# Optimization experiments

Measured on AMD Instinct MI355X. Metric: run time of the kernel, lower is better.

Reference implementation:

```python
import jax, jax.numpy as jnp
import numpy as np

N = 50000       # nodes
E = 1250000     # edges
DIM = 64
H = 16
DPH = DIM // H  # 4
LN_EPS = 1e-5


def setup_inputs() -> dict:
    key = jax.random.key(0)
    ks = jax.random.split(key, 10)
    return {
        "node_feat": jax.random.normal(ks[0], (N, DIM), jnp.float32),
        "edge_feat": jax.random.normal(ks[1], (E, H, DPH), jnp.float32),
        "node_vec": jax.random.normal(ks[2], (N, 3, DIM), jnp.float32),
        "radial": jax.random.uniform(ks[3], (E,), jnp.float32),
        "ln_g": jnp.ones((DIM,), jnp.float32),
        "ln_b": jnp.zeros((DIM,), jnp.float32),
        "qkv_w": jax.random.normal(ks[4], (DIM, 3 * DIM), jnp.float32) / np.sqrt(DIM).astype(np.float32),
        "qkv_b": jnp.zeros((3 * DIM,), jnp.float32),
        "vec_w": jax.random.normal(ks[5], (DIM, 2 * DIM), jnp.float32) / np.sqrt(DIM).astype(np.float32),
        "out_w": jax.random.normal(ks[6], (DIM, 2 * DIM), jnp.float32) / np.sqrt(DIM).astype(np.float32),
        "out_b": jnp.zeros((2 * DIM,), jnp.float32),
        "row": jax.random.randint(ks[7], (E,), 0, N, jnp.int32),
        "col": jax.random.randint(ks[8], (E,), 0, N, jnp.int32),
        "natoms": N,
    }


def reference(node_feat, edge_feat, node_vec, radial, ln_g, ln_b,
              qkv_w, qkv_b, vec_w, out_w, out_b, row, col, natoms):
    # LayerNorm (biased variance, as torch)
    mu = jnp.mean(node_feat, axis=-1, keepdims=True)
    var = jnp.mean(jnp.square(node_feat - mu), axis=-1, keepdims=True)
    x = (node_feat - mu) * jax.lax.rsqrt(var + LN_EPS) * ln_g + ln_b

    # QKV projection -> [N, H, 3*DPH], split
    qkv = (x @ qkv_w + qkv_b).reshape(-1, H, 3 * DPH)
    q = qkv[..., :DPH]
    k = qkv[..., DPH:2 * DPH]
    v = qkv[..., 2 * DPH:]

    # Gather by edge indices, gated dot-product attention per edge  [E, H]
    attn = jax.nn.gelu(jnp.sum(q[row] * k[col], axis=-1), approximate=False) * radial[:, None]

    # Equivariant vector gate  [N, DIM]
    iv = node_vec @ vec_w  # [N, 3, 2*DIM]
    input_dot = jnp.sum(iv[..., :DIM] * iv[..., DIM:], axis=-2)

    # Edge messages and scatter-add into nodes
    m = v[col] * edge_feat * attn[..., None]          # [E, H, DPH]
    m_agg = jax.ops.segment_sum(m, row, num_segments=natoms)  # [N, H, DPH]
    m_agg = m_agg.reshape(natoms, DIM)

    out = m_agg @ out_w + out_b                        # [N, 2*DIM]
    return input_dot * out[..., :DIM] + out[..., DIM:]
```

## Files before the change

### kernel.cpp

```cpp
#include <hip/hip_runtime.h>
#include <math.h>

#define DIM 64
#define NW 4
#define NPB 4
#define CAP 64
#define OVCAP 65536

__device__ __forceinline__ float waveReduceSum(float v) {
    #pragma unroll
    for (int off = 1; off < 64; off <<= 1)
        v += __shfl_xor(v, off, 64);
    return v;
}

__global__ __launch_bounds__(256) void qkv_kernel(
    const float* __restrict__ node_feat,
    const float* __restrict__ ln_g, const float* __restrict__ ln_b,
    const float* __restrict__ qkv_w, const float* __restrict__ qkv_b,
    float* __restrict__ q, float* __restrict__ k, float* __restrict__ v,
    int N)
{
    __shared__ float  wlds[64 * 192];
    __shared__ float4 xs[NW][NPB][16];
    const int wave = threadIdx.x >> 6, lane = threadIdx.x & 63;

    for (int idx = threadIdx.x; idx < 64 * 192; idx += 256) {
        int d = idx / 192, j = idx - d * 192;
        int jj = j & 63, sec = j >> 6;
        int c = 12 * (jj >> 2) + (jj & 3) + 4 * sec;
        wlds[idx] = qkv_w[d * 192 + c];
    }
    const int c0 = 12 * (lane >> 2) + (lane & 3);
    const float b0 = qkv_b[c0], b1 = qkv_b[c0 + 4], b2 = qkv_b[c0 + 8];
    const float gg = ln_g[lane], bb = ln_b[lane];
    __syncthreads();

    const int nstride = gridDim.x * NW * NPB;
    for (int n0 = (blockIdx.x * NW + wave) * NPB; n0 < N; n0 += nstride) {
        const int cnt = min(NPB, N - n0);
        float acc0[NPB], acc1[NPB], acc2[NPB];
        #pragma unroll
        for (int i = 0; i < NPB; ++i) {
            acc0[i] = b0; acc1[i] = b1; acc2[i] = b2;
            if (i < cnt) {
                float nf = node_feat[(size_t)(n0 + i) * DIM + lane];
                float mu = waveReduceSum(nf) * (1.0f / 64.0f);
                float dv = nf - mu;
                float var = waveReduceSum(dv * dv) * (1.0f / 64.0f);
                float x = dv * rsqrtf(var + 1e-5f) * gg + bb;
                ((float*)&xs[wave][i][0])[lane] = x;
            }
        }
        #pragma unroll 4
        for (int d4 = 0; d4 < 16; ++d4) {
            float4 xv[NPB];
            #pragma unroll
            for (int i = 0; i < NPB; ++i) xv[i] = xs[wave][i][d4];
            #pragma unroll
            for (int u = 0; u < 4; ++u) {
                int d = d4 * 4 + u;
                float w0 = wlds[d * 192 + lane];
                float w1 = wlds[d * 192 + lane + 64];
                float w2 = wlds[d * 192 + lane + 128];
                #pragma unroll
                for (int i = 0; i < NPB; ++i) {
                    float xd = (&xv[i].x)[u];
                    acc0[i] = fmaf(xd, w0, acc0[i]);
                    acc1[i] = fmaf(xd, w1, acc1[i]);
                    acc2[i] = fmaf(xd, w2, acc2[i]);
                }
            }
        }
        #pragma unroll
        for (int i = 0; i < NPB; ++i) if (i < cnt) {
            size_t off = (size_t)(n0 + i) * DIM + lane;
            q[off] = acc0[i]; k[off] = acc1[i]; v[off] = acc2[i];
        }
    }
}

__global__ __launch_bounds__(256) void vec_kernel(
    const float* __restrict__ node_vec,
    const float* __restrict__ vec_w,
    float* __restrict__ input_dot,
    float* __restrict__ m_agg,
    int* __restrict__ deg,
    int* __restrict__ ovcnt,
    int N)
{
    __shared__ float  vlds[64 * 128];
    __shared__ float4 nvs[NW][NPB][3][16];
    const int wave = threadIdx.x >> 6, lane = threadIdx.x & 63;

    if (blockIdx.x == 0 && threadIdx.x == 0) *ovcnt = 0;

    for (int idx = threadIdx.x; idx < 64 * 128; idx += 256)
        vlds[idx] = vec_w[idx];
    __syncthreads();

    const int nstride = gridDim.x * NW * NPB;
    for (int n0 = (blockIdx.x * NW + wave) * NPB; n0 < N; n0 += nstride) {
        const int cnt = min(NPB, N - n0);
        float a0[NPB][3], a1[NPB][3];
        #pragma unroll
        for (int i = 0; i < NPB; ++i) {
            #pragma unroll
            for (int s = 0; s < 3; ++s) {
                a0[i][s] = 0.f; a1[i][s] = 0.f;
                if (i < cnt)
                    ((float*)&nvs[wave][i][s][0])[lane] =
                        node_vec[((size_t)(n0 + i) * 3 + s) * DIM + lane];
            }
        }
        #pragma unroll 2
        for (int d4 = 0; d4 < 16; ++d4) {
            #pragma unroll
            for (int u = 0; u < 4; ++u) {
                int d = d4 * 4 + u;
                float w0 = vlds[d * 128 + lane];
                float w1 = vlds[d * 128 + lane + 64];
                #pragma unroll
                for (int i = 0; i < NPB; ++i) {
                    #pragma unroll
                    for (int s = 0; s < 3; ++s) {
                        float nv = ((float*)&nvs[wave][i][s][d4])[u];
                        a0[i][s] = fmaf(nv, w0, a0[i][s]);
                        a1[i][s] = fmaf(nv, w1, a1[i][s]);
                    }
                }
            }
        }
        #pragma unroll
        for (int i = 0; i < NPB; ++i) if (i < cnt) {
            size_t off = (size_t)(n0 + i) * DIM + lane;
            input_dot[off] = a0[i][0] * a1[i][0] + a0[i][1] * a1[i][1]
                           + a0[i][2] * a1[i][2];
            m_agg[off] = 0.0f;
            if (lane == 0) deg[n0 + i] = 0;
        }
    }
}

__global__ __launch_bounds__(256) void scatter_kernel(
    const int* __restrict__ row,
    const int* __restrict__ col,
    int* __restrict__ deg,
    int* __restrict__ perm,
    int* __restrict__ ovcnt,
    int* __restrict__ ovlist,
    const float* __restrict__ q, const float* __restrict__ k,
    const float* __restrict__ v,
    const float* __restrict__ edge_feat, const float* __restrict__ radial,
    float* __restrict__ m_agg,
    int E)
{
    for (int e = blockIdx.x * 256 + threadIdx.x; e < E; e += gridDim.x * 256) {
        int r = row[e];
        int slot = atomicAdd(&deg[r], 1);
        if (slot < CAP) {
            perm[(size_t)r * CAP + slot] = e;
        } else {
            int o = atomicAdd(ovcnt, 1);
            if (o < OVCAP) {
                ovlist[o] = e;
            } else {
                int c = col[e];
                float rad = radial[e];
                float ah[16];
                #pragma unroll
                for (int h = 0; h < 16; ++h) {
                    float p = 0.f;
                    #pragma unroll
                    for (int t = 0; t < 4; ++t)
                        p += q[(size_t)r * DIM + h * 4 + t] *
                             k[(size_t)c * DIM + h * 4 + t];
                    float g = 0.5f * p * (1.0f + erff(p * 0.70710678118654752f));
                    ah[h] = g * rad;
                }
                for (int d = 0; d < DIM; ++d)
                    atomicAdd(&m_agg[(size_t)r * DIM + d],
                              v[(size_t)c * DIM + d] *
                              edge_feat[(size_t)e * DIM + d] * ah[d >> 2]);
            }
        }
    }
}

__global__ __launch_bounds__(256) void agg_kernel(
    const float* __restrict__ q,
    const float* __restrict__ k,
    const float* __restrict__ v,
    const float* __restrict__ edge_feat,
    const float* __restrict__ radial,
    const int* __restrict__ col,
    const int* __restrict__ perm,
    const int* __restrict__ deg,
    float* __restrict__ m_agg,
    int N)
{
    const int wave = threadIdx.x >> 6, lane = threadIdx.x & 63;
    for (int n = blockIdx.x * NW + wave; n < N; n += gridDim.x * NW) {
        int cn = min(deg[n], CAP);
        const int* pr = perm + (size_t)n * CAP;
        const float qd = q[n * DIM + lane];
        float acc = 0.0f;
        #pragma unroll 2
        for (int j = 0; j < cn; ++j) {
            int e = pr[j];
            int c = col[e];
            float kd = k[c * DIM + lane];
            float vd = v[c * DIM + lane];
            float ef = __builtin_nontemporal_load(&edge_feat[e * DIM + lane]);
            float rad = radial[e];
            float p = qd * kd;
            p += __shfl_xor(p, 1, 64);
            p += __shfl_xor(p, 2, 64);
            float g = 0.5f * p * (1.0f + erff(p * 0.70710678118654752f));
            acc = fmaf(vd * ef, g * rad, acc);
        }
        m_agg[n * DIM + lane] += acc;
    }
}

__global__ __launch_bounds__(256) void ovf_kernel(
    const float* __restrict__ q,
    const float* __restrict__ k,
    const float* __restrict__ v,
    const float* __restrict__ edge_feat,
    const float* __restrict__ radial,
    const int* __restrict__ row,
    const int* __restrict__ col,
    const int* __restrict__ ovcnt,
    const int* __restrict__ ovlist,
    float* __restrict__ m_agg)
{
    const int wave = threadIdx.x >> 6, lane = threadIdx.x & 63;
    const int ovn = min(*ovcnt, OVCAP);
    for (int i = blockIdx.x * NW + wave; i < ovn; i += gridDim.x * NW) {
        int e = ovlist[i];
        int r = row[e], c = col[e];
        float p = q[r * DIM + lane] * k[c * DIM + lane];
        p += __shfl_xor(p, 1, 64);
        p += __shfl_xor(p, 2, 64);
        float g = 0.5f * p * (1.0f + erff(p * 0.70710678118654752f));
        float a = g * radial[e];
        float m = v[c * DIM + lane] * edge_feat[(size_t)e * DIM + lane] * a;
        atomicAdd(&m_agg[r * DIM + lane], m);
    }
}

__global__ __launch_bounds__(256) void out_kernel(
    const float* __restrict__ m_agg,
    const float* __restrict__ input_dot,
    const float* __restrict__ out_w,
    const float* __restrict__ out_b,
    float* __restrict__ result,
    int N)
{
    __shared__ float  olds[64 * 128];
    __shared__ float4 ms[NW][NPB][16];
    const int wave = threadIdx.x >> 6, lane = threadIdx.x & 63;

    for (int idx = threadIdx.x; idx < 64 * 128; idx += 256)
        olds[idx] = out_w[idx];
    const float ob0 = out_b[lane], ob1 = out_b[lane + 64];
    __syncthreads();

    const int nstride = gridDim.x * NW * NPB;
    for (int n0 = (blockIdx.x * NW + wave) * NPB; n0 < N; n0 += nstride) {
        const int cnt = min(NPB, N - n0);
        float o0[NPB], o1[NPB];
        #pragma unroll
        for (int i = 0; i < NPB; ++i) {
            o0[i] = ob0; o1[i] = ob1;
            if (i < cnt)
                ((float*)&ms[wave][i][0])[lane] =
                    m_agg[(size_t)(n0 + i) * DIM + lane];
        }
        #pragma unroll 4
        for (int d4 = 0; d4 < 16; ++d4) {
            float4 mv[NPB];
            #pragma unroll
            for (int i = 0; i < NPB; ++i) mv[i] = ms[wave][i][d4];
            #pragma unroll
            for (int u = 0; u < 4; ++u) {
                int d = d4 * 4 + u;
                float w0 = olds[d * 128 + lane];
                float w1 = olds[d * 128 + lane + 64];
                #pragma unroll
                for (int i = 0; i < NPB; ++i) {
                    float md = (&mv[i].x)[u];
                    o0[i] = fmaf(md, w0, o0[i]);
                    o1[i] = fmaf(md, w1, o1[i]);
                }
            }
        }
        #pragma unroll
        for (int i = 0; i < NPB; ++i) if (i < cnt) {
            size_t off = (size_t)(n0 + i) * DIM + lane;
            result[off] = input_dot[off] * o0[i] + o1[i];
        }
    }
}

extern "C" void kernel_launch(void* const* d_in, const int* in_sizes, int n_in,
                              void* d_out, int out_size, void* d_ws, size_t ws_size,
                              hipStream_t stream)
{
    const float* node_feat = (const float*)d_in[0];
    const float* edge_feat = (const float*)d_in[1];
    const float* node_vec  = (const float*)d_in[2];
    const float* radial    = (const float*)d_in[3];
    const float* ln_g      = (const float*)d_in[4];
    const float* ln_b      = (const float*)d_in[5];
    const float* qkv_w     = (const float*)d_in[6];
    const float* qkv_b     = (const float*)d_in[7];
    const float* vec_w     = (const float*)d_in[8];
    const float* out_w     = (const float*)d_in[9];
    const float* out_b     = (const float*)d_in[10];
    const int*   row       = (const int*)d_in[11];
    const int*   col       = (const int*)d_in[12];

    const int N = in_sizes[0] / DIM;
    const int E = in_sizes[3];

    float* ws    = (float*)d_ws;
    float* q     = ws;
    float* k     = q    + (size_t)N * DIM;
    float* v     = k    + (size_t)N * DIM;
    float* idot  = v    + (size_t)N * DIM;
    float* m_agg = idot + (size_t)N * DIM;
    int*   deg    = (int*)(m_agg + (size_t)N * DIM);
    int*   ovcnt  = deg + N;
    int*   ovlist = ovcnt + 1;
    int*   perm   = ovlist + OVCAP;

    const int grid_nodes = 768;
    const int grid_agg   = (N + NW - 1) / NW;

    qkv_kernel<<<grid_nodes, 256, 0, stream>>>(node_feat, ln_g, ln_b,
                                               qkv_w, qkv_b, q, k, v, N);
    vec_kernel<<<grid_nodes, 256, 0, stream>>>(node_vec, vec_w, idot, m_agg,
                                               deg, ovcnt, N);
    scatter_kernel<<<2048, 256, 0, stream>>>(row, col, deg, perm, ovcnt, ovlist,
                                             q, k, v, edge_feat, radial, m_agg, E);
    agg_kernel<<<grid_agg, 256, 0, stream>>>(q, k, v, edge_feat, radial,
                                             col, perm, deg, m_agg, N);
    ovf_kernel<<<256, 256, 0, stream>>>(q, k, v, edge_feat, radial,
                                        row, col, ovcnt, ovlist, m_agg);
    out_kernel<<<grid_nodes, 256, 0, stream>>>(m_agg, idot, out_w, out_b,
                                               (float*)d_out, N);
}
```

Before: 871.3 us.

## Fuse edge bucketing into vec kernel, store (edge,col) pairs, broadcast via shuffles

Moves the degree/overflow reset into the QKV kernel and folds the edge-bucketing scatter into the vec kernel, removing one launch and the m_agg zeroing pass. The bucket list now stores (edge, col) pairs, so the aggregation no longer does a dependent col[] lookup. Each wave preloads its node's pairs and radial values into lanes and broadcasts them with shuffles, replacing serial scalar loads, and writes m_agg directly instead of read-modify-write. The bounded overflow list and its atomic fallback path are dropped, so ovlist is now unbounded and sized by the workspace layout. Per-node bucket storage doubles in size.

```diff
diff --git a/kernel.cpp b/kernel.cpp
--- a/kernel.cpp
+++ b/kernel.cpp
@@ -5,7 +5,6 @@
 #define NW 4
 #define NPB 4
 #define CAP 64
-#define OVCAP 65536
 
 __device__ __forceinline__ float waveReduceSum(float v) {
     #pragma unroll
@@ -19,11 +18,16 @@
     const float* __restrict__ ln_g, const float* __restrict__ ln_b,
     const float* __restrict__ qkv_w, const float* __restrict__ qkv_b,
     float* __restrict__ q, float* __restrict__ k, float* __restrict__ v,
+    int* __restrict__ deg, int* __restrict__ ovcnt,
     int N)
 {
     __shared__ float  wlds[64 * 192];
     __shared__ float4 xs[NW][NPB][16];
     const int wave = threadIdx.x >> 6, lane = threadIdx.x & 63;
+
+    for (int i = blockIdx.x * 256 + threadIdx.x; i < N; i += gridDim.x * 256)
+        deg[i] = 0;
+    if (blockIdx.x == 0 && threadIdx.x == 0) *ovcnt = 0;
 
     for (int idx = threadIdx.x; idx < 64 * 192; idx += 256) {
         int d = idx / 192, j = idx - d * 192;
@@ -84,16 +88,17 @@
     const float* __restrict__ node_vec,
     const float* __restrict__ vec_w,
     float* __restrict__ input_dot,
-    float* __restrict__ m_agg,
+    const int* __restrict__ row,
+    const int* __restrict__ col,
     int* __restrict__ deg,
+    int2* __restrict__ perm2,
     int* __restrict__ ovcnt,
-    int N)
+    int* __restrict__ ovlist,
+    int N, int E)
 {
     __shared__ float  vlds[64 * 128];
     __shared__ float4 nvs[NW][NPB][3][16];
     const int wave = threadIdx.x >> 6, lane = threadIdx.x & 63;
-
-    if (blockIdx.x == 0 && threadIdx.x == 0) *ovcnt = 0;
 
     for (int idx = threadIdx.x; idx < 64 * 128; idx += 256)
         vlds[idx] = vec_w[idx];
@@ -136,53 +141,17 @@
             size_t off = (size_t)(n0 + i) * DIM + lane;
             input_dot[off] = a0[i][0] * a1[i][0] + a0[i][1] * a1[i][1]
                            + a0[i][2] * a1[i][2];
-            m_agg[off] = 0.0f;
-            if (lane == 0) deg[n0 + i] = 0;
-        }
-    }
-}
-
-__global__ __launch_bounds__(256) void scatter_kernel(
-    const int* __restrict__ row,
-    const int* __restrict__ col,
-    int* __restrict__ deg,
-    int* __restrict__ perm,
-    int* __restrict__ ovcnt,
-    int* __restrict__ ovlist,
-    const float* __restrict__ q, const float* __restrict__ k,
-    const float* __restrict__ v,
-    const float* __restrict__ edge_feat, const float* __restrict__ radial,
-    float* __restrict__ m_agg,
-    int E)
-{
+        }
+    }
+
     for (int e = blockIdx.x * 256 + threadIdx.x; e < E; e += gridDim.x * 256) {
         int r = row[e];
         int slot = atomicAdd(&deg[r], 1);
         if (slot < CAP) {
-            perm[(size_t)r * CAP + slot] = e;
+            perm2[(size_t)r * CAP + slot] = make_int2(e, col[e]);
         } else {
             int o = atomicAdd(ovcnt, 1);
-            if (o < OVCAP) {
-                ovlist[o] = e;
-            } else {
-                int c = col[e];
-                float rad = radial[e];
-                float ah[16];
-                #pragma unroll
-                for (int h = 0; h < 16; ++h) {
-                    float p = 0.f;
-                    #pragma unroll
-                    for (int t = 0; t < 4; ++t)
-                        p += q[(size_t)r * DIM + h * 4 + t] *
-                             k[(size_t)c * DIM + h * 4 + t];
-                    float g = 0.5f * p * (1.0f + erff(p * 0.70710678118654752f));
-                    ah[h] = g * rad;
-                }
-                for (int d = 0; d < DIM; ++d)
-                    atomicAdd(&m_agg[(size_t)r * DIM + d],
-                              v[(size_t)c * DIM + d] *
-                              edge_feat[(size_t)e * DIM + d] * ah[d >> 2]);
-            }
+            ovlist[o] = e;
         }
     }
 }
@@ -193,33 +162,38 @@
     const float* __restrict__ v,
     const float* __restrict__ edge_feat,
     const float* __restrict__ radial,
-    const int* __restrict__ col,
-    const int* __restrict__ perm,
+    const int2* __restrict__ perm2,
     const int* __restrict__ deg,
     float* __restrict__ m_agg,
     int N)
 {
     const int wave = threadIdx.x >> 6, lane = threadIdx.x & 63;
     for (int n = blockIdx.x * NW + wave; n < N; n += gridDim.x * NW) {
-        int cn = min(deg[n], CAP);
-        const int* pr = perm + (size_t)n * CAP;
-        const float qd = q[n * DIM + lane];
+        const int cn = min(deg[n], CAP);
+        const int2* pr = perm2 + (size_t)n * CAP;
+        int2 myec = make_int2(0, 0);
+        float myrad = 0.0f;
+        if (lane < cn) {
+            myec = pr[lane];
+            myrad = radial[myec.x];
+        }
+        const float qd = q[(size_t)n * DIM + lane];
         float acc = 0.0f;
-        #pragma unroll 2
+        #pragma unroll 4
         for (int j = 0; j < cn; ++j) {
-            int e = pr[j];
-            int c = col[e];
-            float kd = k[c * DIM + lane];
-            float vd = v[c * DIM + lane];
-            float ef = __builtin_nontemporal_load(&edge_feat[e * DIM + lane]);
-            float rad = radial[e];
+            int   e   = __shfl(myec.x, j, 64);
+            int   c   = __shfl(myec.y, j, 64);
+            float rad = __shfl(myrad, j, 64);
+            float kd = k[(size_t)c * DIM + lane];
+            float vd = v[(size_t)c * DIM + lane];
+            float ef = __builtin_nontemporal_load(&edge_feat[(size_t)e * DIM + lane]);
             float p = qd * kd;
             p += __shfl_xor(p, 1, 64);
             p += __shfl_xor(p, 2, 64);
             float g = 0.5f * p * (1.0f + erff(p * 0.70710678118654752f));
             acc = fmaf(vd * ef, g * rad, acc);
         }
-        m_agg[n * DIM + lane] += acc;
+        m_agg[(size_t)n * DIM + lane] = acc;
     }
 }
 
@@ -236,17 +210,17 @@
     float* __restrict__ m_agg)
 {
     const int wave = threadIdx.x >> 6, lane = threadIdx.x & 63;
-    const int ovn = min(*ovcnt, OVCAP);
+    const int ovn = *ovcnt;
     for (int i = blockIdx.x * NW + wave; i < ovn; i += gridDim.x * NW) {
         int e = ovlist[i];
         int r = row[e], c = col[e];
-        float p = q[r * DIM + lane] * k[c * DIM + lane];
+        float p = q[(size_t)r * DIM + lane] * k[(size_t)c * DIM + lane];
         p += __shfl_xor(p, 1, 64);
         p += __shfl_xor(p, 2, 64);
         float g = 0.5f * p * (1.0f + erff(p * 0.70710678118654752f));
         float a = g * radial[e];
-        float m = v[c * DIM + lane] * edge_feat[(size_t)e * DIM + lane] * a;
-        atomicAdd(&m_agg[r * DIM + lane], m);
+        float m = v[(size_t)c * DIM + lane] * edge_feat[(size_t)e * DIM + lane] * a;
+        atomicAdd(&m_agg[(size_t)r * DIM + lane], m);
     }
 }
 
@@ -331,22 +305,22 @@
     float* v     = k    + (size_t)N * DIM;
     float* idot  = v    + (size_t)N * DIM;
     float* m_agg = idot + (size_t)N * DIM;
-    int*   deg    = (int*)(m_agg + (size_t)N * DIM);
+    int2*  perm2  = (int2*)(m_agg + (size_t)N * DIM);
+    int*   deg    = (int*)(perm2 + (size_t)N * CAP);
     int*   ovcnt  = deg + N;
     int*   ovlist = ovcnt + 1;
-    int*   perm   = ovlist + OVCAP;
 
     const int grid_nodes = 768;
     const int grid_agg   = (N + NW - 1) / NW;
 
     qkv_kernel<<<grid_nodes, 256, 0, stream>>>(node_feat, ln_g, ln_b,
-                                               qkv_w, qkv_b, q, k, v, N);
-    vec_kernel<<<grid_nodes, 256, 0, stream>>>(node_vec, vec_w, idot, m_agg,
+                                               qkv_w, qkv_b, q, k, v,
                                                deg, ovcnt, N);
-    scatter_kernel<<<2048, 256, 0, stream>>>(row, col, deg, perm, ovcnt, ovlist,
-                                             q, k, v, edge_feat, radial, m_agg, E);
+    vec_kernel<<<grid_nodes, 256, 0, stream>>>(node_vec, vec_w, idot,
+                                               row, col, deg, perm2,
+                                               ovcnt, ovlist, N, E);
     agg_kernel<<<grid_agg, 256, 0, stream>>>(q, k, v, edge_feat, radial,
-                                             col, perm, deg, m_agg, N);
+                                             perm2, deg, m_agg, N);
     ovf_kernel<<<256, 256, 0, stream>>>(q, k, v, edge_feat, radial,
                                         row, col, ovcnt, ovlist, m_agg);
     out_kernel<<<grid_nodes, 256, 0, stream>>>(m_agg, idot, out_w, out_b,
```

Result: faster. 734.1 us (-15.7%).
